# Kernel tuning notes

Hardware: AMD Instinct MI355X
Metric: run time of the kernel (lower is better)

The kernel has to match this reference:

```python
import jax, jax.numpy as jnp
import numpy as np

BATCH, TIME, IN, HID = 32, 512, 512, 1024
THRESHOLD = 1.0
BETA = 1.0 / 2.0  # 1/tau


def setup_inputs() -> dict:
    key = jax.random.key(0)
    kx, kw, kb = jax.random.split(key, 3)
    x = jax.random.normal(kx, (BATCH, TIME, IN), dtype=jnp.float32)
    bound = 1.0 / np.sqrt(IN)  # nn.Linear default init range
    W = jax.random.uniform(kw, (HID, IN), minval=-bound, maxval=bound, dtype=jnp.float32)
    b = jax.random.uniform(kb, (HID,), minval=-bound, maxval=bound, dtype=jnp.float32)
    return {"x": x, "W": W, "b": b}


def reference(x, W, b):
    # Precompute all per-step linear projections in one big GEMM: [B,T,H]
    hidden = jnp.einsum("bti,hi->bth", x, W) + b

    def step(mem, h_t):
        # h_t: [B,H]
        mem = BETA * mem + h_t
        spk = (mem > THRESHOLD).astype(h_t.dtype)
        mem = mem * (1.0 - spk)  # hard reset
        return mem, spk

    mem0 = jnp.zeros((x.shape[0], W.shape[0]), dtype=x.dtype)
    # scan over time: [T,B,H]
    _, spikes = jax.lax.scan(step, mem0, jnp.swapaxes(hidden, 0, 1))
    return jnp.swapaxes(spikes, 0, 1)  # [B,T,H]
```

## Files before the change

kernel.cpp:

```cpp
#include <hip/hip_runtime.h>

#define BATCH 32
#define TIME  512
#define INF   512
#define HIDF  1024

#define MBT  128
#define NBH  128
#define KCH  16
#define NCH  (INF / KCH)
#define TILEF (MBT * KCH)

#define GLD16(g, l) __builtin_amdgcn_global_load_lds(                      \
    (const __attribute__((address_space(1))) void*)(g),                    \
    (__attribute__((address_space(3))) void*)(l), 16, 0, 0)

__global__ __launch_bounds__(256, 3)
void snn_gemm_seqfma(const float* __restrict__ x, const float* __restrict__ W,
                     const float* __restrict__ bias, float* __restrict__ hidden) {
    __shared__ __align__(16) float xs[2 * TILEF];
    __shared__ __align__(16) float ws[2 * TILEF];

    const int tid = threadIdx.x;
    const int l   = tid & 63;
    const int wv  = __builtin_amdgcn_readfirstlane(tid >> 6);
    const int lx  = l & 7;
    const int ly  = (l >> 3) & 7;
    const int bt0 = blockIdx.y * MBT;
    const int h0  = blockIdx.x * NBH;
    const int wbt = 64 * (wv >> 1);
    const int wh  = 64 * (wv & 1);

    const int rl   = l >> 2;
    const int qs   = l & 3;
    const int rowA = 32 * wv + rl;
    const int rowB = rowA + 16;
    const int qA   = qs ^ ((rowA >> 3) & 3);
    const int qB   = qs ^ ((rowB >> 3) & 3);
    const float* xgA = x + (size_t)(bt0 + rowA) * INF + qA * 4;
    const float* xgB = x + (size_t)(bt0 + rowB) * INF + qB * 4;
    const float* wgA = W + (size_t)(h0 + rowA) * INF + qA * 4;
    const float* wgB = W + (size_t)(h0 + rowB) * INF + qB * 4;
    const int dOffA = (32 * wv) * KCH;
    const int dOffB = dOffA + 16 * KCH;

    GLD16(xgA, xs + dOffA);
    GLD16(xgB, xs + dOffB);
    GLD16(wgA, ws + dOffA);
    GLD16(wgB, ws + dOffB);

    float acc[8][8];
    #pragma unroll
    for (int r = 0; r < 8; ++r)
        #pragma unroll
        for (int c = 0; c < 8; ++c) acc[r][c] = 0.0f;

    __syncthreads();

    for (int kc = 0; kc < NCH; ++kc) {
        const int p  = kc & 1;
        const int np = p ^ 1;

        if (kc + 1 < NCH) {
            const int so = (kc + 1) * KCH;
            float* xd = xs + np * TILEF;
            float* wd = ws + np * TILEF;
            GLD16(xgA + so, xd + dOffA);
            GLD16(xgB + so, xd + dOffB);
            GLD16(wgA + so, wd + dOffA);
            GLD16(wgB + so, wd + dOffB);
        }

        const float* xb = xs + p * TILEF;
        const float* wb = ws + p * TILEF;
        #pragma unroll
        for (int g = 0; g < 4; ++g) {
            const int gx_ = (g ^ (ly & 3)) * 4;
            const int gw_ = (g ^ (lx & 3)) * 4;
            float4 xf[8], wf[8];
            #pragma unroll
            for (int r = 0; r < 8; ++r)
                xf[r] = *(const float4*)(xb + (wbt + ly * 8 + r) * KCH + gx_);
            #pragma unroll
            for (int c = 0; c < 8; ++c)
                wf[c] = *(const float4*)(wb + (wh + lx * 8 + c) * KCH + gw_);
            #pragma unroll
            for (int r = 0; r < 8; ++r)
                #pragma unroll
                for (int c = 0; c < 8; ++c)
                    acc[r][c] = __fmaf_rn(xf[r].x, wf[c].x, acc[r][c]);
            #pragma unroll
            for (int r = 0; r < 8; ++r)
                #pragma unroll
                for (int c = 0; c < 8; ++c)
                    acc[r][c] = __fmaf_rn(xf[r].y, wf[c].y, acc[r][c]);
            #pragma unroll
            for (int r = 0; r < 8; ++r)
                #pragma unroll
                for (int c = 0; c < 8; ++c)
                    acc[r][c] = __fmaf_rn(xf[r].z, wf[c].z, acc[r][c]);
            #pragma unroll
            for (int r = 0; r < 8; ++r)
                #pragma unroll
                for (int c = 0; c < 8; ++c)
                    acc[r][c] = __fmaf_rn(xf[r].w, wf[c].w, acc[r][c]);
        }
        __syncthreads();
    }

    float bv[8];
    #pragma unroll
    for (int c = 0; c < 8; ++c) bv[c] = bias[h0 + wh + lx * 8 + c];
    #pragma unroll
    for (int r = 0; r < 8; ++r) {
        float* orow = hidden + (size_t)(bt0 + wbt + ly * 8 + r) * HIDF
                             + h0 + wh + lx * 8;
        float4 o0, o1;
        o0.x = __fadd_rn(acc[r][0], bv[0]);
        o0.y = __fadd_rn(acc[r][1], bv[1]);
        o0.z = __fadd_rn(acc[r][2], bv[2]);
        o0.w = __fadd_rn(acc[r][3], bv[3]);
        o1.x = __fadd_rn(acc[r][4], bv[4]);
        o1.y = __fadd_rn(acc[r][5], bv[5]);
        o1.z = __fadd_rn(acc[r][6], bv[6]);
        o1.w = __fadd_rn(acc[r][7], bv[7]);
        ((float4*)orow)[0] = o0;
        ((float4*)orow)[1] = o1;
    }
}

__global__ __launch_bounds__(256)
void snn_scan_np(float* __restrict__ io) {
    const int n = blockIdx.x * 256 + threadIdx.x;
    const int b = n >> 10;
    const int h = n & 1023;
    float* p = io + (size_t)b * TIME * HIDF + h;

    float mem = 0.0f;
    for (int tb = 0; tb < TIME / 64; ++tb) {
        float hv[64];
        #pragma unroll
        for (int u = 0; u < 64; ++u) hv[u] = p[(size_t)(tb * 64 + u) * HIDF];
        float sp[64];
        #pragma unroll
        for (int u = 0; u < 64; ++u) {
            mem = __fadd_rn(__fmul_rn(0.5f, mem), hv[u]);
            bool s = mem > 1.0f;
            sp[u] = s ? 1.0f : 0.0f;
            if (s) mem = 0.0f;
        }
        #pragma unroll
        for (int u = 0; u < 64; ++u) p[(size_t)(tb * 64 + u) * HIDF] = sp[u];
    }
}

extern "C" void kernel_launch(void* const* d_in, const int* in_sizes, int n_in,
                              void* d_out, int out_size, void* d_ws, size_t ws_size,
                              hipStream_t stream) {
    const float* x    = (const float*)d_in[0];
    const float* W    = (const float*)d_in[1];
    const float* bias = (const float*)d_in[2];
    float* out = (float*)d_out;

    dim3 g1(HIDF / NBH, (BATCH * TIME) / MBT);
    snn_gemm_seqfma<<<g1, 256, 0, stream>>>(x, W, bias, out);

    snn_scan_np<<<(BATCH * HIDF) / 256, 256, 0, stream>>>(out);
}
```

Before: 327.9 us.

## Interleave GEMM thread-to-row mapping with new LDS swizzle, shrink scan blocks

The GEMM now assigns each thread strided rows and columns (ly + 8*r, lx + 8*c) instead of contiguous 8x8 blocks, and changes the LDS XOR swizzle key to match, so reads of shared memory avoid bank conflicts and output stores coalesce across lanes. The epilogue now writes scalar floats strided by 8 instead of float4 pairs. The scan kernel drops to 64-thread blocks to spread waves across more CUs. The trade-off is more, narrower store instructions in exchange for better coalescing and fewer LDS conflicts.

```diff
diff --git a/kernel.cpp b/kernel.cpp
--- a/kernel.cpp
+++ b/kernel.cpp
@@ -32,15 +32,13 @@
     const int wh  = 64 * (wv & 1);
 
     const int rl   = l >> 2;
-    const int qs   = l & 3;
+    const int qs   = (l & 3) ^ ((rl >> 1) & 3);
     const int rowA = 32 * wv + rl;
     const int rowB = rowA + 16;
-    const int qA   = qs ^ ((rowA >> 3) & 3);
-    const int qB   = qs ^ ((rowB >> 3) & 3);
-    const float* xgA = x + (size_t)(bt0 + rowA) * INF + qA * 4;
-    const float* xgB = x + (size_t)(bt0 + rowB) * INF + qB * 4;
-    const float* wgA = W + (size_t)(h0 + rowA) * INF + qA * 4;
-    const float* wgB = W + (size_t)(h0 + rowB) * INF + qB * 4;
+    const float* xgA = x + (size_t)(bt0 + rowA) * INF + qs * 4;
+    const float* xgB = x + (size_t)(bt0 + rowB) * INF + qs * 4;
+    const float* wgA = W + (size_t)(h0 + rowA) * INF + qs * 4;
+    const float* wgB = W + (size_t)(h0 + rowB) * INF + qs * 4;
     const int dOffA = (32 * wv) * KCH;
     const int dOffB = dOffA + 16 * KCH;
 
@@ -54,6 +52,9 @@
     for (int r = 0; r < 8; ++r)
         #pragma unroll
         for (int c = 0; c < 8; ++c) acc[r][c] = 0.0f;
+
+    const int keyx = (ly >> 1) & 3;
+    const int keyw = (lx >> 1) & 3;
 
     __syncthreads();
 
@@ -71,19 +72,19 @@
             GLD16(wgB + so, wd + dOffB);
         }
 
-        const float* xb = xs + p * TILEF;
-        const float* wb = ws + p * TILEF;
+        const float* xrow = xs + p * TILEF + (wbt + ly) * KCH;
+        const float* wrow = ws + p * TILEF + (wh  + lx) * KCH;
         #pragma unroll
         for (int g = 0; g < 4; ++g) {
-            const int gx_ = (g ^ (ly & 3)) * 4;
-            const int gw_ = (g ^ (lx & 3)) * 4;
+            const float* xg_ = xrow + (g ^ keyx) * 4;
+            const float* wg_ = wrow + (g ^ keyw) * 4;
             float4 xf[8], wf[8];
             #pragma unroll
             for (int r = 0; r < 8; ++r)
-                xf[r] = *(const float4*)(xb + (wbt + ly * 8 + r) * KCH + gx_);
+                xf[r] = *(const float4*)(xg_ + r * 8 * KCH);
             #pragma unroll
             for (int c = 0; c < 8; ++c)
-                wf[c] = *(const float4*)(wb + (wh + lx * 8 + c) * KCH + gw_);
+                wf[c] = *(const float4*)(wg_ + c * 8 * KCH);
             #pragma unroll
             for (int r = 0; r < 8; ++r)
                 #pragma unroll
@@ -110,28 +111,20 @@
 
     float bv[8];
     #pragma unroll
-    for (int c = 0; c < 8; ++c) bv[c] = bias[h0 + wh + lx * 8 + c];
+    for (int c = 0; c < 8; ++c) bv[c] = bias[h0 + wh + lx + 8 * c];
     #pragma unroll
     for (int r = 0; r < 8; ++r) {
-        float* orow = hidden + (size_t)(bt0 + wbt + ly * 8 + r) * HIDF
-                             + h0 + wh + lx * 8;
-        float4 o0, o1;
-        o0.x = __fadd_rn(acc[r][0], bv[0]);
-        o0.y = __fadd_rn(acc[r][1], bv[1]);
-        o0.z = __fadd_rn(acc[r][2], bv[2]);
-        o0.w = __fadd_rn(acc[r][3], bv[3]);
-        o1.x = __fadd_rn(acc[r][4], bv[4]);
-        o1.y = __fadd_rn(acc[r][5], bv[5]);
-        o1.z = __fadd_rn(acc[r][6], bv[6]);
-        o1.w = __fadd_rn(acc[r][7], bv[7]);
-        ((float4*)orow)[0] = o0;
-        ((float4*)orow)[1] = o1;
+        float* orow = hidden + (size_t)(bt0 + wbt + ly + 8 * r) * HIDF
+                             + h0 + wh + lx;
+        #pragma unroll
+        for (int c = 0; c < 8; ++c)
+            orow[8 * c] = __fadd_rn(acc[r][c], bv[c]);
     }
 }
 
-__global__ __launch_bounds__(256)
+__global__ __launch_bounds__(64)
 void snn_scan_np(float* __restrict__ io) {
-    const int n = blockIdx.x * 256 + threadIdx.x;
+    const int n = blockIdx.x * 64 + threadIdx.x;
     const int b = n >> 10;
     const int h = n & 1023;
     float* p = io + (size_t)b * TIME * HIDF + h;
@@ -165,5 +158,5 @@
     dim3 g1(HIDF / NBH, (BATCH * TIME) / MBT);
     snn_gemm_seqfma<<<g1, 256, 0, stream>>>(x, W, bias, out);
 
-    snn_scan_np<<<(BATCH * HIDF) / 256, 256, 0, stream>>>(out);
+    snn_scan_np<<<(BATCH * HIDF) / 64, 64, 0, stream>>>(out);
 }
```

Measured after the change: 327.9 us. No clear change (+0.0%).
